# Optimization experiments

Measured on AMD Instinct MI355X. Metric: run time of the kernel, lower is better.

## Reference

```python
import jax, jax.numpy as jnp
import numpy as np

B, S, D = 4, 4096, 2048

def setup_inputs() -> dict:
    key = jax.random.key(0)
    k1, k2 = jax.random.split(key)
    k = jax.random.normal(k1, (B, S, D), dtype=jnp.float32)
    v = jax.random.normal(k2, (B, S, D), dtype=jnp.float32)
    kv_state = jnp.zeros((D, D), dtype=jnp.float32)
    k_sum = jnp.zeros((D,), dtype=jnp.float32)
    return {"k": k, "v": v, "kv_state": kv_state, "k_sum": k_sum}

def reference(k, v, kv_state, k_sum):
    b, s, d = k.shape
    k_flat = k.reshape(-1, d)  # (N, D), N = B*S
    v_flat = v.reshape(-1, d)
    # Accumulate outer-product state: kv_state += sum_i k_i v_i^T
    kv_new = kv_state + jnp.einsum('nd,ne->de', k_flat, v_flat)
    ks_new = k_sum + k_flat.sum(axis=0)
    # Readout: context = k @ kv_state^T ; normalizer = k @ k_sum
    context = jnp.einsum('nd,ed->ne', k_flat, kv_new).reshape(b, s, d)
    normalizer = (k_flat @ ks_new).reshape(b, s, 1)
    return context, normalizer
```

## Files before the change

### kernel.cpp

```cpp
#include <hip/hip_runtime.h>
#include <hip/hip_bf16.h>
#include <cstdio>
#include <cstdint>

#define NBIG 16384
#define DDIM 2048
#define SPLITK 4

#define BM 256
#define BN 256
#define BKT 64

typedef __attribute__((ext_vector_type(4))) float f32x4;
typedef __attribute__((ext_vector_type(8))) short bf16x8;

__device__ __forceinline__ unsigned short f2bf(float f) {
  union { float f; unsigned u; } v; v.f = f;
  return (unsigned short)((v.u + 0x7FFFu + ((v.u >> 16) & 1u)) >> 16);
}

__device__ __forceinline__ void gll16(const void* g, void* l) {
  auto gp = reinterpret_cast<const __attribute__((address_space(1))) unsigned int*>(
      reinterpret_cast<uintptr_t>(g));
  auto lp = reinterpret_cast<__attribute__((address_space(3))) unsigned int*>(
      (unsigned int)reinterpret_cast<uintptr_t>(l));
  __builtin_amdgcn_global_load_lds(gp, lp, 16, 0, 0);
}

__device__ __forceinline__ void waitvm8() { asm volatile("s_waitcnt vmcnt(8)" ::: "memory"); }
__device__ __forceinline__ void waitvm0() { asm volatile("s_waitcnt vmcnt(0)" ::: "memory"); }
__device__ __forceinline__ void barrier_pinned() {
  __builtin_amdgcn_sched_barrier(0);
  __builtin_amdgcn_s_barrier();
  __builtin_amdgcn_sched_barrier(0);
}

__device__ __forceinline__ void xcd_swizzle(int& bx, int& by, int& bz) {
  const unsigned nx = gridDim.x, ny = gridDim.y;
  const unsigned nwg = nx * ny * gridDim.z;
  unsigned wg = blockIdx.x + nx * (blockIdx.y + ny * blockIdx.z);
  wg = (wg & 7u) * (nwg >> 3) + (wg >> 3);
  bx = wg % nx;
  unsigned r = wg / nx;
  by = r % ny;
  bz = r / ny;
}

__global__ __launch_bounds__(256) void prep_kernel(
    const float* __restrict__ k, const float* __restrict__ v,
    unsigned short* __restrict__ KT, unsigned short* __restrict__ VT,
    unsigned short* __restrict__ Kbf, float* __restrict__ ks)
{
  __shared__ unsigned short sm[64][66];
  __shared__ float sks[64];
  const int t = threadIdx.x;
  const int tiles_d = DDIM / 64;
  const int n0 = (blockIdx.x / tiles_d) * 64;
  const int d0 = (blockIdx.x % tiles_d) * 64;
  const bool is_k = (blockIdx.y == 0);
  const float* __restrict__ src = is_k ? k : v;
  unsigned short* __restrict__ dstT = is_k ? KT : VT;

  const int r = t >> 4;
  const int c = (t & 15) * 4;

  if (t < 64) sks[t] = 0.f;
  __syncthreads();

  float a0 = 0.f, a1 = 0.f, a2 = 0.f, a3 = 0.f;
#pragma unroll
  for (int i = 0; i < 4; ++i) {
    const int row = i * 16 + r;
    f32x4 val = *reinterpret_cast<const f32x4*>(&src[(size_t)(n0 + row) * DDIM + d0 + c]);
    unsigned short b0 = f2bf(val.x), b1 = f2bf(val.y), b2 = f2bf(val.z), b3 = f2bf(val.w);
    sm[row][c + 0] = b0; sm[row][c + 1] = b1;
    sm[row][c + 2] = b2; sm[row][c + 3] = b3;
    if (is_k) {
      unsigned int p0 = (unsigned)b0 | ((unsigned)b1 << 16);
      unsigned int p1 = (unsigned)b2 | ((unsigned)b3 << 16);
      *reinterpret_cast<uint2*>(&Kbf[(size_t)(n0 + row) * DDIM + d0 + c]) = make_uint2(p0, p1);
      a0 += val.x; a1 += val.y; a2 += val.z; a3 += val.w;
    }
  }
  if (is_k) {
    atomicAdd(&sks[c + 0], a0);
    atomicAdd(&sks[c + 1], a1);
    atomicAdd(&sks[c + 2], a2);
    atomicAdd(&sks[c + 3], a3);
  }
  __syncthreads();

#pragma unroll
  for (int i = 0; i < 4; ++i) {
    const int rowp = i * 16 + r;
    unsigned int p0 = (unsigned)sm[c + 0][rowp] | ((unsigned)sm[c + 1][rowp] << 16);
    unsigned int p1 = (unsigned)sm[c + 2][rowp] | ((unsigned)sm[c + 3][rowp] << 16);
    *reinterpret_cast<uint2*>(&dstT[(size_t)(d0 + rowp) * NBIG + n0 + c]) = make_uint2(p0, p1);
  }
  if (is_k && t < 64) atomicAdd(&ks[d0 + t], sks[t]);
}

__global__ void init_ks_kernel(const float* __restrict__ ksum, float* __restrict__ ks) {
  int i = blockIdx.x * 256 + threadIdx.x;
  if (i < DDIM) ks[i] = ksum[i];
}

__global__ __launch_bounds__(512, 2) void gemm256_kernel(
    const unsigned short* __restrict__ A, const unsigned short* __restrict__ B,
    float* __restrict__ C, int lda, int ldb, int kchunk, long long zstride)
{
  __shared__ unsigned short Abuf[2][BM * BKT];
  __shared__ unsigned short Bbuf[2][BN * BKT];

  int bx, by, bz;
  xcd_swizzle(bx, by, bz);

  const int t = threadIdx.x, lane = t & 63, w = t >> 6;
  const int wm = w >> 2, wn = w & 3;
  const int m0 = by * BM, n0 = bx * BN;
  const int kbeg = bz * kchunk;
  const int NT = kchunk / BKT;

  const int srow = lane >> 3;
  const int sgr  = (lane & 7) ^ srow;
  const unsigned short* Ag = A + (size_t)(m0 + srow) * lda + kbeg + sgr * 8;
  const unsigned short* Bg = B + (size_t)(n0 + srow) * ldb + kbeg + sgr * 8;

  const int hi = lane >> 4;
  const int lo7 = lane & 7;
  const int swz0 = ((0 + hi) ^ lo7) * 8;
  const int swz1 = ((4 + hi) ^ lo7) * 8;
  const int arow = (wm * 128 + (lane & 15)) * BKT;
  const int brow = (wn * 64 + (lane & 15)) * BKT;

  auto stage_op = [&](const unsigned short* G, unsigned short* Lbase, int ld_,
                      int kt, int half) {
    const unsigned short* g = G + (size_t)(half * 128 + w * 16) * ld_ + (size_t)kt * BKT;
    unsigned short* l = Lbase + (half * 128 + w * 16) * BKT;
    gll16(g, l);
    gll16(g + (size_t)8 * ld_, l + 8 * BKT);
  };

  stage_op(Bg, Bbuf[0], ldb, 0, 0); stage_op(Bg, Bbuf[0], ldb, 0, 1);
  stage_op(Ag, Abuf[0], lda, 0, 0); stage_op(Ag, Abuf[0], lda, 0, 1);
  stage_op(Bg, Bbuf[1], ldb, 1, 0); stage_op(Bg, Bbuf[1], ldb, 1, 1);
  stage_op(Ag, Abuf[1], lda, 1, 0); stage_op(Ag, Abuf[1], lda, 1, 1);
  waitvm8();
  __builtin_amdgcn_s_barrier();
  __builtin_amdgcn_sched_barrier(0);

  f32x4 acc[8][4] = {};

#pragma unroll 2
  for (int tl = 0; tl < NT; ++tl) {
    const int q = tl & 1;
    const unsigned short* Al = Abuf[q];
    const unsigned short* Bl = Bbuf[q];
    bf16x8 af[4][2], bA[2][2], bB[2][2];

#pragma unroll
    for (int m = 0; m < 4; ++m) {
      af[m][0] = *reinterpret_cast<const bf16x8*>(Al + arow + m * 16 * BKT + swz0);
      af[m][1] = *reinterpret_cast<const bf16x8*>(Al + arow + m * 16 * BKT + swz1);
    }
#pragma unroll
    for (int n = 0; n < 2; ++n) {
      bA[n][0] = *reinterpret_cast<const bf16x8*>(Bl + brow + n * 16 * BKT + swz0);
      bA[n][1] = *reinterpret_cast<const bf16x8*>(Bl + brow + n * 16 * BKT + swz1);
    }
    __builtin_amdgcn_s_setprio(1);
#pragma unroll
    for (int m = 0; m < 4; ++m)
#pragma unroll
      for (int n = 0; n < 2; ++n) {
        acc[m][n] = __builtin_amdgcn_mfma_f32_16x16x32_bf16(af[m][0], bA[n][0], acc[m][n], 0, 0, 0);
        acc[m][n] = __builtin_amdgcn_mfma_f32_16x16x32_bf16(af[m][1], bA[n][1], acc[m][n], 0, 0, 0);
      }
    __builtin_amdgcn_s_setprio(0);

#pragma unroll
    for (int n = 0; n < 2; ++n) {
      bB[n][0] = *reinterpret_cast<const bf16x8*>(Bl + brow + (32 + n * 16) * BKT + swz0);
      bB[n][1] = *reinterpret_cast<const bf16x8*>(Bl + brow + (32 + n * 16) * BKT + swz1);
    }
    __builtin_amdgcn_s_setprio(1);
#pragma unroll
    for (int m = 0; m < 4; ++m)
#pragma unroll
      for (int n = 0; n < 2; ++n) {
        acc[m][2 + n] = __builtin_amdgcn_mfma_f32_16x16x32_bf16(af[m][0], bB[n][0], acc[m][2 + n], 0, 0, 0);
        acc[m][2 + n] = __builtin_amdgcn_mfma_f32_16x16x32_bf16(af[m][1], bB[n][1], acc[m][2 + n], 0, 0, 0);
      }
    __builtin_amdgcn_s_setprio(0);
    barrier_pinned();

    if (tl + 2 < NT) {
      stage_op(Bg, Bbuf[q], ldb, tl + 2, 0);
      stage_op(Bg, Bbuf[q], ldb, tl + 2, 1);
    }
#pragma unroll
    for (int m = 0; m < 4; ++m) {
      af[m][0] = *reinterpret_cast<const bf16x8*>(Al + arow + (64 + m * 16) * BKT + swz0);
      af[m][1] = *reinterpret_cast<const bf16x8*>(Al + arow + (64 + m * 16) * BKT + swz1);
    }
    __builtin_amdgcn_s_setprio(1);
#pragma unroll
    for (int m = 0; m < 4; ++m)
#pragma unroll
      for (int n = 0; n < 2; ++n) {
        acc[4 + m][n] = __builtin_amdgcn_mfma_f32_16x16x32_bf16(af[m][0], bA[n][0], acc[4 + m][n], 0, 0, 0);
        acc[4 + m][n] = __builtin_amdgcn_mfma_f32_16x16x32_bf16(af[m][1], bA[n][1], acc[4 + m][n], 0, 0, 0);
      }
    __builtin_amdgcn_s_setprio(0);
    barrier_pinned();

    if (tl + 2 < NT) {
      stage_op(Ag, Abuf[q], lda, tl + 2, 0);
      stage_op(Ag, Abuf[q], lda, tl + 2, 1);
    }
    __builtin_amdgcn_s_setprio(1);
#pragma unroll
    for (int m = 0; m < 4; ++m)
#pragma unroll
      for (int n = 0; n < 2; ++n) {
        acc[4 + m][2 + n] = __builtin_amdgcn_mfma_f32_16x16x32_bf16(af[m][0], bB[n][0], acc[4 + m][2 + n], 0, 0, 0);
        acc[4 + m][2 + n] = __builtin_amdgcn_mfma_f32_16x16x32_bf16(af[m][1], bB[n][1], acc[4 + m][2 + n], 0, 0, 0);
      }
    __builtin_amdgcn_s_setprio(0);
    if (tl + 1 < NT) {
      if (tl + 2 < NT) waitvm8();
      else             waitvm0();
      __builtin_amdgcn_s_barrier();
      __builtin_amdgcn_sched_barrier(0);
    }
  }

  float* Cz = C + (size_t)bz * zstride;
  const int crow0 = m0 + wm * 128 + hi * 4;
  const int ccol0 = n0 + wn * 64 + (lane & 15);
#pragma unroll
  for (int m = 0; m < 8; ++m)
#pragma unroll
    for (int n = 0; n < 4; ++n)
#pragma unroll
      for (int j = 0; j < 4; ++j)
        Cz[(size_t)(crow0 + m * 16 + j) * DDIM + ccol0 + n * 16] = acc[m][n][j];
}

__global__ __launch_bounds__(256) void kvconv_kernel(
    const float* __restrict__ kvp, const float* __restrict__ kvst,
    unsigned short* __restrict__ kvbf)
{
  size_t i = ((size_t)blockIdx.x * 256 + threadIdx.x) * 4;
  f32x4 s = *reinterpret_cast<const f32x4*>(&kvst[i]);
#pragma unroll
  for (int z = 0; z < SPLITK; ++z) {
    f32x4 p = *reinterpret_cast<const f32x4*>(&kvp[(size_t)z * DDIM * DDIM + i]);
    s.x += p.x; s.y += p.y; s.z += p.z; s.w += p.w;
  }
  unsigned int p0 = (unsigned)f2bf(s.x) | ((unsigned)f2bf(s.y) << 16);
  unsigned int p1 = (unsigned)f2bf(s.z) | ((unsigned)f2bf(s.w) << 16);
  *reinterpret_cast<uint2*>(&kvbf[i]) = make_uint2(p0, p1);
}

__global__ __launch_bounds__(256) void norm_kernel(
    const unsigned short* __restrict__ Kbf, const float* __restrict__ ks,
    float* __restrict__ out)
{
  const int lane = threadIdx.x & 63;
  const int w = threadIdx.x >> 6;
  const int row = blockIdx.x * 4 + w;
  const unsigned short* kr = Kbf + (size_t)row * DDIM;
  float s = 0.f;
#pragma unroll
  for (int i = 0; i < 4; ++i) {
    bf16x8 a = *reinterpret_cast<const bf16x8*>(&kr[i * 512 + lane * 8]);
    f32x4 b0 = *reinterpret_cast<const f32x4*>(&ks[i * 512 + lane * 8]);
    f32x4 b1 = *reinterpret_cast<const f32x4*>(&ks[i * 512 + lane * 8 + 4]);
    float af[8];
#pragma unroll
    for (int j = 0; j < 8; ++j) {
      union { unsigned u; float f; } cv;
      cv.u = ((unsigned)(unsigned short)a[j]) << 16;
      af[j] = cv.f;
    }
    s += af[0] * b0.x + af[1] * b0.y + af[2] * b0.z + af[3] * b0.w
       + af[4] * b1.x + af[5] * b1.y + af[6] * b1.z + af[7] * b1.w;
  }
  for (int off = 32; off; off >>= 1) s += __shfl_down(s, off, 64);
  if (lane == 0) out[row] = s;
}

extern "C" void kernel_launch(void* const* d_in, const int* in_sizes, int n_in,
                              void* d_out, int out_size, void* d_ws, size_t ws_size,
                              hipStream_t stream) {
  const float* k    = (const float*)d_in[0];
  const float* v    = (const float*)d_in[1];
  const float* kvst = (const float*)d_in[2];
  const float* ksum = (const float*)d_in[3];

  const size_t SZ_T = (size_t)DDIM * NBIG * 2;
  const size_t WS_NEED = SZ_T * 3 + (size_t)DDIM * DDIM * 2 + DDIM * 4;
  if (ws_size < WS_NEED) {
    fprintf(stderr, "kernel_launch: ws too small %zu < %zu\n", ws_size, WS_NEED);
    return;
  }
  char* ws = (char*)d_ws;
  unsigned short* KT   = (unsigned short*)ws;
  unsigned short* VT   = (unsigned short*)(ws + SZ_T);
  unsigned short* Kbf  = (unsigned short*)(ws + 2 * SZ_T);
  unsigned short* KVbf = (unsigned short*)(ws + 3 * SZ_T);
  float* ks            = (float*)(ws + 3 * SZ_T + (size_t)DDIM * DDIM * 2);

  float* ctx = (float*)d_out;
  float* nrm = ctx + (size_t)NBIG * DDIM;
  float* kvp = ctx;

  init_ks_kernel<<<(DDIM + 255) / 256, 256, 0, stream>>>(ksum, ks);
  prep_kernel<<<dim3((NBIG / 64) * (DDIM / 64), 2), 256, 0, stream>>>(k, v, KT, VT, Kbf, ks);
  gemm256_kernel<<<dim3(DDIM / BN, DDIM / BM, SPLITK), 512, 0, stream>>>(
      KT, VT, kvp, NBIG, NBIG, NBIG / SPLITK, (long long)DDIM * DDIM);
  kvconv_kernel<<<(DDIM * DDIM) / (256 * 4), 256, 0, stream>>>(kvp, kvst, KVbf);
  gemm256_kernel<<<dim3(DDIM / BN, NBIG / BM, 1), 512, 0, stream>>>(
      Kbf, KVbf, ctx, DDIM, DDIM, DDIM, 0);
  norm_kernel<<<NBIG / 4, 256, 0, stream>>>(Kbf, ks, nrm);
}
```

Baseline: 383.7 us.

## Load full A/B fragments up front and merge prefetch into single barrier phase

Measured after the change: 386.1 us. No clear change (+0.6%).

```diff
diff --git a/kernel.cpp b/kernel.cpp
--- a/kernel.cpp
+++ b/kernel.cpp
@@ -29,6 +29,7 @@
 
 __device__ __forceinline__ void waitvm8() { asm volatile("s_waitcnt vmcnt(8)" ::: "memory"); }
 __device__ __forceinline__ void waitvm0() { asm volatile("s_waitcnt vmcnt(0)" ::: "memory"); }
+__device__ __forceinline__ void waitlgkm0() { asm volatile("s_waitcnt lgkmcnt(0)" ::: "memory"); }
 __device__ __forceinline__ void barrier_pinned() {
   __builtin_amdgcn_sched_barrier(0);
   __builtin_amdgcn_s_barrier();
@@ -156,80 +157,54 @@
     const int q = tl & 1;
     const unsigned short* Al = Abuf[q];
     const unsigned short* Bl = Bbuf[q];
-    bf16x8 af[4][2], bA[2][2], bB[2][2];
-
-#pragma unroll
-    for (int m = 0; m < 4; ++m) {
+    const bool pf = (tl + 2 < NT);
+    bf16x8 af[8][2], bb[4][2];
+
+#pragma unroll
+    for (int m = 0; m < 8; ++m) {
       af[m][0] = *reinterpret_cast<const bf16x8*>(Al + arow + m * 16 * BKT + swz0);
       af[m][1] = *reinterpret_cast<const bf16x8*>(Al + arow + m * 16 * BKT + swz1);
     }
 #pragma unroll
-    for (int n = 0; n < 2; ++n) {
-      bA[n][0] = *reinterpret_cast<const bf16x8*>(Bl + brow + n * 16 * BKT + swz0);
-      bA[n][1] = *reinterpret_cast<const bf16x8*>(Bl + brow + n * 16 * BKT + swz1);
-    }
+    for (int n = 0; n < 4; ++n) {
+      bb[n][0] = *reinterpret_cast<const bf16x8*>(Bl + brow + n * 16 * BKT + swz0);
+      bb[n][1] = *reinterpret_cast<const bf16x8*>(Bl + brow + n * 16 * BKT + swz1);
+    }
+
     __builtin_amdgcn_s_setprio(1);
 #pragma unroll
-    for (int m = 0; m < 4; ++m)
-#pragma unroll
-      for (int n = 0; n < 2; ++n) {
-        acc[m][n] = __builtin_amdgcn_mfma_f32_16x16x32_bf16(af[m][0], bA[n][0], acc[m][n], 0, 0, 0);
-        acc[m][n] = __builtin_amdgcn_mfma_f32_16x16x32_bf16(af[m][1], bA[n][1], acc[m][n], 0, 0, 0);
-      }
+    for (int kk = 0; kk < 2; ++kk)
+#pragma unroll
+      for (int m = 0; m < 4; ++m)
+#pragma unroll
+        for (int n = 0; n < 4; ++n)
+          acc[m][n] = __builtin_amdgcn_mfma_f32_16x16x32_bf16(af[m][kk], bb[n][kk], acc[m][n], 0, 0, 0);
     __builtin_amdgcn_s_setprio(0);
 
-#pragma unroll
-    for (int n = 0; n < 2; ++n) {
-      bB[n][0] = *reinterpret_cast<const bf16x8*>(Bl + brow + (32 + n * 16) * BKT + swz0);
-      bB[n][1] = *reinterpret_cast<const bf16x8*>(Bl + brow + (32 + n * 16) * BKT + swz1);
-    }
-    __builtin_amdgcn_s_setprio(1);
-#pragma unroll
-    for (int m = 0; m < 4; ++m)
-#pragma unroll
-      for (int n = 0; n < 2; ++n) {
-        acc[m][2 + n] = __builtin_amdgcn_mfma_f32_16x16x32_bf16(af[m][0], bB[n][0], acc[m][2 + n], 0, 0, 0);
-        acc[m][2 + n] = __builtin_amdgcn_mfma_f32_16x16x32_bf16(af[m][1], bB[n][1], acc[m][2 + n], 0, 0, 0);
-      }
-    __builtin_amdgcn_s_setprio(0);
+    waitlgkm0();
     barrier_pinned();
 
-    if (tl + 2 < NT) {
+    if (pf) {
       stage_op(Bg, Bbuf[q], ldb, tl + 2, 0);
       stage_op(Bg, Bbuf[q], ldb, tl + 2, 1);
-    }
-#pragma unroll
-    for (int m = 0; m < 4; ++m) {
-      af[m][0] = *reinterpret_cast<const bf16x8*>(Al + arow + (64 + m * 16) * BKT + swz0);
-      af[m][1] = *reinterpret_cast<const bf16x8*>(Al + arow + (64 + m * 16) * BKT + swz1);
-    }
-    __builtin_amdgcn_s_setprio(1);
-#pragma unroll
-    for (int m = 0; m < 4; ++m)
-#pragma unroll
-      for (int n = 0; n < 2; ++n) {
-        acc[4 + m][n] = __builtin_amdgcn_mfma_f32_16x16x32_bf16(af[m][0], bA[n][0], acc[4 + m][n], 0, 0, 0);
-        acc[4 + m][n] = __builtin_amdgcn_mfma_f32_16x16x32_bf16(af[m][1], bA[n][1], acc[4 + m][n], 0, 0, 0);
-      }
-    __builtin_amdgcn_s_setprio(0);
-    barrier_pinned();
-
-    if (tl + 2 < NT) {
       stage_op(Ag, Abuf[q], lda, tl + 2, 0);
       stage_op(Ag, Abuf[q], lda, tl + 2, 1);
     }
+
     __builtin_amdgcn_s_setprio(1);
 #pragma unroll
-    for (int m = 0; m < 4; ++m)
-#pragma unroll
-      for (int n = 0; n < 2; ++n) {
-        acc[4 + m][2 + n] = __builtin_amdgcn_mfma_f32_16x16x32_bf16(af[m][0], bB[n][0], acc[4 + m][2 + n], 0, 0, 0);
-        acc[4 + m][2 + n] = __builtin_amdgcn_mfma_f32_16x16x32_bf16(af[m][1], bB[n][1], acc[4 + m][2 + n], 0, 0, 0);
-      }
+    for (int kk = 0; kk < 2; ++kk)
+#pragma unroll
+      for (int m = 4; m < 8; ++m)
+#pragma unroll
+        for (int n = 0; n < 4; ++n)
+          acc[m][n] = __builtin_amdgcn_mfma_f32_16x16x32_bf16(af[m][kk], bb[n][kk], acc[m][n], 0, 0, 0);
     __builtin_amdgcn_s_setprio(0);
+    __builtin_amdgcn_sched_barrier(0);
+
     if (tl + 1 < NT) {
-      if (tl + 2 < NT) waitvm8();
-      else             waitvm0();
+      if (pf) waitvm8();
+      else    waitvm0();
       __builtin_amdgcn_s_barrier();
       __builtin_amdgcn_sched_barrier(0);
     }
```
